# Kernel tuning notes

Hardware: AMD Instinct MI355X
Metric: run time of the kernel (lower is better)

Reference implementation:

```python
import jax, jax.numpy as jnp
import numpy as np

N = 8192          # mesh vertices
E = 49152         # directed edges (avg degree 6)
M = 25            # kernel_size per pseudo-dim
DIM = 3           # pseudo-coordinate dim
K = M ** DIM      # 15625 weight matrices per layer
S = 2 ** DIM      # 8 nonzero degree-1 B-spline products per edge
LC, UC = -0.22703196, 0.36853024   # curvature range
LM, UM = 1.2585511, 1.648841       # myelin range
R = 10.0
LAYER_DIMS = [(2, 32), (32, 64), (64, 64), (64, 32), (32, 1)]


def transform(x):
    # rescale curv/myelin channels into [-R, R] with clamping (matches torch masking)
    t0 = (x[:, 0] - LC) / (UC - LC) * (2.0 * R) - R
    t1 = (x[:, 1] - LM) / (UM - LM) * (2.0 * R) - R
    return jnp.stack([jnp.clip(t0, -R, R), jnp.clip(t1, -R, R)], axis=1)


def spline_basis(pseudo):
    # open B-spline, degree 1: v in [0, M-1); 8 corner products per edge
    v = pseudo * (M - 1)
    lo = jnp.floor(v)
    f = v - lo                                                    # [E, DIM]
    lo = lo.astype(jnp.int32)
    bits = (jnp.arange(S)[:, None] >> jnp.arange(DIM)[None, :]) & 1   # [S, DIM]
    oh = bits.astype(pseudo.dtype)
    basis = jnp.prod(oh[None] * f[:, None, :] + (1.0 - oh[None]) * (1.0 - f[:, None, :]), axis=-1)  # [E, S]
    strides = (M ** jnp.arange(DIM)).astype(jnp.int32)
    wi = jnp.sum((lo[:, None, :] + bits[None]) * strides[None, None, :], axis=-1)  # [E, S] kernel indices
    return basis, wi


def spline_conv(h, src, dst, basis, wi, W, root, bias):
    xj = h[src]                                             # [E, Fin] gather
    msg = jnp.zeros((xj.shape[0], W.shape[2]), h.dtype)
    for s in range(S):                                      # fixed 8-way basis loop
        msg = msg + basis[:, s, None] * jnp.einsum('ei,eio->eo', xj, W[wi[:, s]])
    agg = jax.ops.segment_sum(msg, dst, num_segments=N)     # scatter-sum (norm=False)
    return agg + h @ root + bias


def setup_inputs() -> dict:
    key = jax.random.key(0)
    ks = jax.random.split(key, 3 + 2 * len(LAYER_DIMS))
    inp = {
        "x": jax.random.normal(ks[0], (N, 2), dtype=jnp.float32),
        "edge_index": jax.random.randint(ks[1], (2, E), 0, N),
        "pseudo": jax.random.uniform(ks[2], (E, DIM), dtype=jnp.float32),
    }
    for i, (fi, fo) in enumerate(LAYER_DIMS):
        kw, kr = ks[3 + 2 * i], ks[4 + 2 * i]
        inp[f"W{i+1}"] = jax.random.normal(kw, (K, fi, fo), dtype=jnp.float32) / np.float32(np.sqrt(fi * S))
        inp[f"root{i+1}"] = jax.random.normal(kr, (fi, fo), dtype=jnp.float32) / np.float32(np.sqrt(fi))
        inp[f"b{i+1}"] = jnp.zeros((fo,), dtype=jnp.float32)
    return inp


def reference(x, edge_index, pseudo, W1, root1, b1, W2, root2, b2, W3, root3, b3,
              W4, root4, b4, W5, root5, b5):
    src, dst = edge_index[0], edge_index[1]
    basis, wi = spline_basis(pseudo)   # shared across all 5 layers, as in the torch model
    h = transform(x)
    for W, r, b in ((W1, root1, b1), (W2, root2, b2), (W3, root3, b3),
                    (W4, root4, b4), (W5, root5, b5)):
        h = jax.nn.elu(spline_conv(h, src, dst, basis, wi, W, r, b))
    return h.reshape(-1)
```

## Files before the change

### kernel.cpp

```cpp
#include <hip/hip_runtime.h>
#include <math.h>

#define NV 8192
#define EV 49152
#define KK 15625

typedef __attribute__((ext_vector_type(8))) short bf16x8;
typedef __attribute__((ext_vector_type(4))) float f32x4;

__device__ __forceinline__ unsigned short bf16rne(float x) {
    unsigned u = __float_as_uint(x);
    unsigned r = u + 0x7FFFu + ((u >> 16) & 1u);
    return (unsigned short)(r >> 16);
}
__device__ __forceinline__ float bf16tof(unsigned short h) {
    return __uint_as_float(((unsigned)h) << 16);
}

__device__ __forceinline__ void edge_frac(const float* __restrict__ pseudo, int e,
                                          float f[3], int lo[3]) {
#pragma unroll
    for (int j = 0; j < 3; ++j) {
        float v = pseudo[e * 3 + j] * 24.0f;
        float fl = floorf(v);
        int l = (int)fl;
        l = l < 0 ? 0 : (l > 23 ? 23 : l);
        lo[j] = l;
        f[j] = v - (float)l;
    }
}

__global__ void transform_kernel(const float* __restrict__ x, float* __restrict__ h0) {
    int n = blockIdx.x * blockDim.x + threadIdx.x;
    if (n >= NV) return;
    const float LC = -0.22703196f, UC = 0.36853024f;
    const float LM = 1.2585511f, UM = 1.648841f;
    const float R = 10.0f;
    float t0 = (x[n * 2 + 0] - LC) / (UC - LC) * (2.0f * R) - R;
    float t1 = (x[n * 2 + 1] - LM) / (UM - LM) * (2.0f * R) - R;
    h0[n * 2 + 0] = fminf(fmaxf(t0, -R), R);
    h0[n * 2 + 1] = fminf(fmaxf(t1, -R), R);
}

__global__ void hist_kernel(const float* __restrict__ pseudo, int* __restrict__ counts) {
    int e = blockIdx.x * blockDim.x + threadIdx.x;
    if (e >= EV) return;
    float f[3]; int lo[3];
    edge_frac(pseudo, e, f, lo);
#pragma unroll
    for (int s = 0; s < 8; ++s) {
        int wi = (lo[0] + (s & 1)) + 25 * (lo[1] + ((s >> 1) & 1)) + 625 * (lo[2] + ((s >> 2) & 1));
        atomicAdd(&counts[wi], 1);
    }
}

__global__ void scan_kernel(const int* __restrict__ counts, int* __restrict__ offsets,
                            int* __restrict__ cursor) {
    __shared__ int sums[256];
    const int CH = 62;
    int t = threadIdx.x;
    int base = t * CH;
    int s = 0;
    for (int i = 0; i < CH; ++i) {
        int idx = base + i;
        if (idx < KK) s += counts[idx];
    }
    sums[t] = s;
    __syncthreads();
    for (int d = 1; d < 256; d <<= 1) {
        int v = (t >= d) ? sums[t - d] : 0;
        __syncthreads();
        sums[t] += v;
        __syncthreads();
    }
    int run = (t > 0) ? sums[t - 1] : 0;
    for (int i = 0; i < CH; ++i) {
        int idx = base + i;
        if (idx < KK) {
            offsets[idx] = run;
            cursor[idx] = run;
            run += counts[idx];
        }
    }
    if (t == 255) offsets[KK] = run;
}

__global__ void scatter_kernel(const float* __restrict__ pseudo, const int* __restrict__ ei,
                               int* __restrict__ cursor,
                               int2* __restrict__ pair_sb, int* __restrict__ pair_dst) {
    int e = blockIdx.x * blockDim.x + threadIdx.x;
    if (e >= EV) return;
    float f[3]; int lo[3];
    edge_frac(pseudo, e, f, lo);
    int src = ei[e];
    int dst = ei[EV + e];
#pragma unroll
    for (int s = 0; s < 8; ++s) {
        float b = ((s & 1) ? f[0] : 1.0f - f[0]) *
                  (((s >> 1) & 1) ? f[1] : 1.0f - f[1]) *
                  (((s >> 2) & 1) ? f[2] : 1.0f - f[2]);
        int wi = (lo[0] + (s & 1)) + 25 * (lo[1] + ((s >> 1) & 1)) + 625 * (lo[2] + ((s >> 2) & 1));
        int pos = atomicAdd(&cursor[wi], 1);
        pair_sb[pos] = make_int2(src, __float_as_int(b));
        pair_dst[pos] = dst;
    }
}

template <int FIN, int FOUT>
__global__ __launch_bounds__(256) void conv_mfma(
    const float* __restrict__ h, const float* __restrict__ W,
    const int* __restrict__ offsets, const int2* __restrict__ pair_sb,
    const int* __restrict__ pair_dst, float* __restrict__ agg) {
    constexpr int KT = FIN / 32;
    constexpr int NT = FOUT / 16;
    int w = threadIdx.x >> 6;
    int lane = threadIdx.x & 63;
    int k = blockIdx.x * 4 + w;
    if (k >= KK) return;
    int start = offsets[k];
    int n = offsets[k + 1] - start;
    if (n <= 0) return;
    int l15 = lane & 15;
    int lg = lane >> 4;

    const float* Wk = W + (size_t)k * (FIN * FOUT);
    bf16x8 Bh[NT][KT], Bl[NT][KT];
#pragma unroll
    for (int n0 = 0; n0 < NT; ++n0)
#pragma unroll
        for (int k0 = 0; k0 < KT; ++k0)
#pragma unroll
            for (int i = 0; i < 8; ++i) {
                float wv = Wk[(size_t)(k0 * 32 + lg * 8 + i) * FOUT + n0 * 16 + l15];
                unsigned short hi = bf16rne(wv);
                unsigned short lo = bf16rne(wv - bf16tof(hi));
                Bh[n0][k0][i] = (short)hi;
                Bl[n0][k0][i] = (short)lo;
            }

    for (int m0 = 0; m0 < n; m0 += 16) {
        int ra = m0 + l15;
        bool va = ra < n;
        int2 sb = pair_sb[start + (va ? ra : 0)];
        float b = va ? __int_as_float(sb.y) : 0.0f;
        const float* xr = h + (size_t)sb.x * FIN + lg * 8;

        f32x4 acc[NT];
#pragma unroll
        for (int n0 = 0; n0 < NT; ++n0) acc[n0] = (f32x4){0.f, 0.f, 0.f, 0.f};

#pragma unroll
        for (int k0 = 0; k0 < KT; ++k0) {
            float4 v0 = *(const float4*)(xr + k0 * 32);
            float4 v1 = *(const float4*)(xr + k0 * 32 + 4);
            float xv[8] = {v0.x * b, v0.y * b, v0.z * b, v0.w * b,
                           v1.x * b, v1.y * b, v1.z * b, v1.w * b};
            bf16x8 Ah, Al;
#pragma unroll
            for (int i = 0; i < 8; ++i) {
                unsigned short hi = bf16rne(xv[i]);
                unsigned short lo = bf16rne(xv[i] - bf16tof(hi));
                Ah[i] = (short)hi;
                Al[i] = (short)lo;
            }
#pragma unroll
            for (int n0 = 0; n0 < NT; ++n0) {
                acc[n0] = __builtin_amdgcn_mfma_f32_16x16x32_bf16(Ah, Bh[n0][k0], acc[n0], 0, 0, 0);
                acc[n0] = __builtin_amdgcn_mfma_f32_16x16x32_bf16(Ah, Bl[n0][k0], acc[n0], 0, 0, 0);
                acc[n0] = __builtin_amdgcn_mfma_f32_16x16x32_bf16(Al, Bh[n0][k0], acc[n0], 0, 0, 0);
            }
        }

#pragma unroll
        for (int j = 0; j < 4; ++j) {
            int rm = m0 + lg * 4 + j;
            if (rm < n) {
                int d = pair_dst[start + rm];
#pragma unroll
                for (int n0 = 0; n0 < NT; ++n0)
                    atomicAdd(&agg[(size_t)d * FOUT + n0 * 16 + l15], acc[n0][j]);
            }
        }
    }
}

__global__ __launch_bounds__(256) void conv_l1(
    const float* __restrict__ h, const float* __restrict__ W,
    const int* __restrict__ offsets, const int2* __restrict__ pair_sb,
    const int* __restrict__ pair_dst, float* __restrict__ agg) {
    int w = threadIdx.x >> 6;
    int lane = threadIdx.x & 63;
    int k = blockIdx.x * 4 + w;
    if (k >= KK) return;
    int start = offsets[k];
    int n = offsets[k + 1] - start;
    if (n <= 0) return;
    int o = lane & 31;
    int g = lane >> 5;
    const float* Wk = W + (size_t)k * 64;
    float w0 = Wk[o], w1 = Wk[32 + o];
    const float2* h2 = (const float2*)h;
    for (int r = g; r < n; r += 2) {
        int2 sb = pair_sb[start + r];
        float b = __int_as_float(sb.y);
        int dst = pair_dst[start + r];
        float2 xv = h2[sb.x];
        atomicAdd(&agg[(size_t)dst * 32 + o], b * (xv.x * w0 + xv.y * w1));
    }
}

__global__ __launch_bounds__(256) void conv_f1(
    const float* __restrict__ h, const float* __restrict__ W,
    const int* __restrict__ offsets, const int2* __restrict__ pair_sb,
    const int* __restrict__ pair_dst, float* __restrict__ agg) {
    int w = threadIdx.x >> 6;
    int lane = threadIdx.x & 63;
    int k = blockIdx.x * 4 + w;
    if (k >= KK) return;
    int start = offsets[k];
    int n = offsets[k + 1] - start;
    if (n <= 0) return;
    int i = lane & 31;
    int g = lane >> 5;
    float wk = W[(size_t)k * 32 + i];
    for (int r = g; r < n; r += 2) {
        int2 sb = pair_sb[start + r];
        float b = __int_as_float(sb.y);
        int dst = pair_dst[start + r];
        float val = h[(size_t)sb.x * 32 + i] * wk * b;
#pragma unroll
        for (int d = 16; d >= 1; d >>= 1) val += __shfl_xor(val, d, 32);
        if (i == 0) atomicAdd(&agg[dst], val);
    }
}

template <int FIN, int FOUT>
__global__ void node_kernel(const float* __restrict__ h, const float* __restrict__ agg,
                            const float* __restrict__ root, const float* __restrict__ bias,
                            float* __restrict__ hout) {
    int idx = blockIdx.x * blockDim.x + threadIdx.x;
    if (idx >= NV * FOUT) return;
    int n = idx / FOUT, o = idx % FOUT;
    float acc = agg[idx] + bias[o];
#pragma unroll
    for (int i = 0; i < FIN; ++i) acc += h[n * FIN + i] * root[i * FOUT + o];
    hout[idx] = acc > 0.0f ? acc : expm1f(acc);
}

extern "C" void kernel_launch(void* const* d_in, const int* in_sizes, int n_in,
                              void* d_out, int out_size, void* d_ws, size_t ws_size,
                              hipStream_t stream) {
    const float* x      = (const float*)d_in[0];
    const int*   ei     = (const int*)d_in[1];
    const float* pseudo = (const float*)d_in[2];
    const float* W1 = (const float*)d_in[3];
    const float* r1 = (const float*)d_in[4];
    const float* b1 = (const float*)d_in[5];
    const float* W2 = (const float*)d_in[6];
    const float* r2 = (const float*)d_in[7];
    const float* b2 = (const float*)d_in[8];
    const float* W3 = (const float*)d_in[9];
    const float* r3 = (const float*)d_in[10];
    const float* b3 = (const float*)d_in[11];
    const float* W4 = (const float*)d_in[12];
    const float* r4 = (const float*)d_in[13];
    const float* b4 = (const float*)d_in[14];
    const float* W5 = (const float*)d_in[15];
    const float* r5 = (const float*)d_in[16];
    const float* b5 = (const float*)d_in[17];

    char* ws = (char*)d_ws;
    size_t off = 0;
    auto alloc = [&](size_t bytes) {
        void* p = ws + off;
        off += (bytes + 255) & ~(size_t)255;
        return p;
    };
    int*   counts   = (int*)alloc(KK * sizeof(int));
    int*   offsets  = (int*)alloc((KK + 1) * sizeof(int));
    int*   cursor   = (int*)alloc(KK * sizeof(int));
    int2*  pair_sb  = (int2*)alloc((size_t)EV * 8 * sizeof(int2));
    int*   pair_dst = (int*)alloc((size_t)EV * 8 * sizeof(int));
    float* hA       = (float*)alloc((size_t)NV * 64 * sizeof(float));
    float* hB       = (float*)alloc((size_t)NV * 64 * sizeof(float));
    float* agg      = (float*)alloc((size_t)NV * 64 * sizeof(float));

    const int CGRID = (KK + 3) / 4;

    hipMemsetAsync(counts, 0, KK * sizeof(int), stream);
    transform_kernel<<<(NV + 255) / 256, 256, 0, stream>>>(x, hA);
    hist_kernel<<<(EV + 255) / 256, 256, 0, stream>>>(pseudo, counts);
    scan_kernel<<<1, 256, 0, stream>>>(counts, offsets, cursor);
    scatter_kernel<<<(EV + 255) / 256, 256, 0, stream>>>(pseudo, ei, cursor, pair_sb, pair_dst);

    hipMemsetAsync(agg, 0, (size_t)NV * 32 * sizeof(float), stream);
    conv_l1<<<CGRID, 256, 0, stream>>>(hA, W1, offsets, pair_sb, pair_dst, agg);
    node_kernel<2, 32><<<(NV * 32 + 255) / 256, 256, 0, stream>>>(hA, agg, r1, b1, hB);

    hipMemsetAsync(agg, 0, (size_t)NV * 64 * sizeof(float), stream);
    conv_mfma<32, 64><<<CGRID, 256, 0, stream>>>(hB, W2, offsets, pair_sb, pair_dst, agg);
    node_kernel<32, 64><<<(NV * 64 + 255) / 256, 256, 0, stream>>>(hB, agg, r2, b2, hA);

    hipMemsetAsync(agg, 0, (size_t)NV * 64 * sizeof(float), stream);
    conv_mfma<64, 64><<<CGRID, 256, 0, stream>>>(hA, W3, offsets, pair_sb, pair_dst, agg);
    node_kernel<64, 64><<<(NV * 64 + 255) / 256, 256, 0, stream>>>(hA, agg, r3, b3, hB);

    hipMemsetAsync(agg, 0, (size_t)NV * 32 * sizeof(float), stream);
    conv_mfma<64, 32><<<CGRID, 256, 0, stream>>>(hB, W4, offsets, pair_sb, pair_dst, agg);
    node_kernel<64, 32><<<(NV * 32 + 255) / 256, 256, 0, stream>>>(hB, agg, r4, b4, hA);

    hipMemsetAsync(agg, 0, (size_t)NV * sizeof(float), stream);
    conv_f1<<<CGRID, 256, 0, stream>>>(hA, W5, offsets, pair_sb, pair_dst, agg);
    node_kernel<32, 1><<<(NV + 255) / 256, 256, 0, stream>>>(hA, agg, r5, b5, (float*)d_out);
}
```

Baseline: 509.9 us.

## Split conv output columns across waves and fold agg zeroing into kernels

Each MFMA conv wave now handles one 16-column output slice of a kernel matrix, so the work for one weight matrix spreads over several waves. Per-wave register use drops and more waves are in flight, at the cost of each wave reloading the same source rows and pair lists. The memsets are removed: a prep kernel zeroes counts and agg alongside the transform, and each node kernel clears agg after reading it. This cuts launch count but makes every node kernel touch the full 64-wide agg buffer.

New measurement: 518.9 us. No clear change (+1.8%).

```diff
diff --git a/kernel.cpp b/kernel.cpp
--- a/kernel.cpp
+++ b/kernel.cpp
@@ -30,16 +30,20 @@
     }
 }
 
-__global__ void transform_kernel(const float* __restrict__ x, float* __restrict__ h0) {
-    int n = blockIdx.x * blockDim.x + threadIdx.x;
-    if (n >= NV) return;
-    const float LC = -0.22703196f, UC = 0.36853024f;
-    const float LM = 1.2585511f, UM = 1.648841f;
-    const float R = 10.0f;
-    float t0 = (x[n * 2 + 0] - LC) / (UC - LC) * (2.0f * R) - R;
-    float t1 = (x[n * 2 + 1] - LM) / (UM - LM) * (2.0f * R) - R;
-    h0[n * 2 + 0] = fminf(fmaxf(t0, -R), R);
-    h0[n * 2 + 1] = fminf(fmaxf(t1, -R), R);
+__global__ void prep_kernel(const float* __restrict__ x, float* __restrict__ h0,
+                            int* __restrict__ counts, float* __restrict__ agg) {
+    int gt = blockIdx.x * blockDim.x + threadIdx.x;
+    if (gt < NV) {
+        const float LC = -0.22703196f, UC = 0.36853024f;
+        const float LM = 1.2585511f, UM = 1.648841f;
+        const float R = 10.0f;
+        float t0 = (x[gt * 2 + 0] - LC) / (UC - LC) * (2.0f * R) - R;
+        float t1 = (x[gt * 2 + 1] - LM) / (UM - LM) * (2.0f * R) - R;
+        h0[gt * 2 + 0] = fminf(fmaxf(t0, -R), R);
+        h0[gt * 2 + 1] = fminf(fmaxf(t1, -R), R);
+    }
+    if (gt < KK) counts[gt] = 0;
+    if (gt < NV * 64) agg[gt] = 0.0f;
 }
 
 __global__ void hist_kernel(const float* __restrict__ pseudo, int* __restrict__ counts) {
@@ -107,15 +111,17 @@
 }
 
 template <int FIN, int FOUT>
-__global__ __launch_bounds__(256) void conv_mfma(
+__global__ __launch_bounds__(256) void conv_v5(
     const float* __restrict__ h, const float* __restrict__ W,
     const int* __restrict__ offsets, const int2* __restrict__ pair_sb,
     const int* __restrict__ pair_dst, float* __restrict__ agg) {
     constexpr int KT = FIN / 32;
     constexpr int NT = FOUT / 16;
+    constexpr int BPB = 4 / NT;
     int w = threadIdx.x >> 6;
     int lane = threadIdx.x & 63;
-    int k = blockIdx.x * 4 + w;
+    int nslice = w % NT;
+    int k = blockIdx.x * BPB + w / NT;
     if (k >= KK) return;
     int start = offsets[k];
     int n = offsets[k + 1] - start;
@@ -123,32 +129,30 @@
     int l15 = lane & 15;
     int lg = lane >> 4;
 
-    const float* Wk = W + (size_t)k * (FIN * FOUT);
-    bf16x8 Bh[NT][KT], Bl[NT][KT];
-#pragma unroll
-    for (int n0 = 0; n0 < NT; ++n0)
-#pragma unroll
-        for (int k0 = 0; k0 < KT; ++k0)
-#pragma unroll
-            for (int i = 0; i < 8; ++i) {
-                float wv = Wk[(size_t)(k0 * 32 + lg * 8 + i) * FOUT + n0 * 16 + l15];
-                unsigned short hi = bf16rne(wv);
-                unsigned short lo = bf16rne(wv - bf16tof(hi));
-                Bh[n0][k0][i] = (short)hi;
-                Bl[n0][k0][i] = (short)lo;
-            }
+    const float* Wk = W + (size_t)k * (FIN * FOUT) + nslice * 16 + l15;
+    bf16x8 Bh[KT], Bl[KT];
+#pragma unroll
+    for (int k0 = 0; k0 < KT; ++k0)
+#pragma unroll
+        for (int i = 0; i < 8; ++i) {
+            float wv = Wk[(size_t)(k0 * 32 + lg * 8 + i) * FOUT];
+            unsigned short hi = bf16rne(wv);
+            unsigned short lo = bf16rne(wv - bf16tof(hi));
+            Bh[k0][i] = (short)hi;
+            Bl[k0][i] = (short)lo;
+        }
+
+    const int2* psb = pair_sb + start;
+    const int* pdst = pair_dst + start;
 
     for (int m0 = 0; m0 < n; m0 += 16) {
         int ra = m0 + l15;
         bool va = ra < n;
-        int2 sb = pair_sb[start + (va ? ra : 0)];
+        int2 sb = psb[va ? ra : 0];
         float b = va ? __int_as_float(sb.y) : 0.0f;
         const float* xr = h + (size_t)sb.x * FIN + lg * 8;
 
-        f32x4 acc[NT];
-#pragma unroll
-        for (int n0 = 0; n0 < NT; ++n0) acc[n0] = (f32x4){0.f, 0.f, 0.f, 0.f};
-
+        f32x4 acc = (f32x4){0.f, 0.f, 0.f, 0.f};
 #pragma unroll
         for (int k0 = 0; k0 < KT; ++k0) {
             float4 v0 = *(const float4*)(xr + k0 * 32);
@@ -163,22 +167,17 @@
                 Ah[i] = (short)hi;
                 Al[i] = (short)lo;
             }
-#pragma unroll
-            for (int n0 = 0; n0 < NT; ++n0) {
-                acc[n0] = __builtin_amdgcn_mfma_f32_16x16x32_bf16(Ah, Bh[n0][k0], acc[n0], 0, 0, 0);
-                acc[n0] = __builtin_amdgcn_mfma_f32_16x16x32_bf16(Ah, Bl[n0][k0], acc[n0], 0, 0, 0);
-                acc[n0] = __builtin_amdgcn_mfma_f32_16x16x32_bf16(Al, Bh[n0][k0], acc[n0], 0, 0, 0);
-            }
+            acc = __builtin_amdgcn_mfma_f32_16x16x32_bf16(Ah, Bh[k0], acc, 0, 0, 0);
+            acc = __builtin_amdgcn_mfma_f32_16x16x32_bf16(Ah, Bl[k0], acc, 0, 0, 0);
+            acc = __builtin_amdgcn_mfma_f32_16x16x32_bf16(Al, Bh[k0], acc, 0, 0, 0);
         }
 
 #pragma unroll
         for (int j = 0; j < 4; ++j) {
             int rm = m0 + lg * 4 + j;
             if (rm < n) {
-                int d = pair_dst[start + rm];
-#pragma unroll
-                for (int n0 = 0; n0 < NT; ++n0)
-                    atomicAdd(&agg[(size_t)d * FOUT + n0 * 16 + l15], acc[n0][j]);
+                int d = pdst[rm];
+                atomicAdd(&agg[(size_t)d * FOUT + nslice * 16 + l15], acc[j]);
             }
         }
     }
@@ -235,16 +234,19 @@
 }
 
 template <int FIN, int FOUT>
-__global__ void node_kernel(const float* __restrict__ h, const float* __restrict__ agg,
+__global__ void node_kernel(const float* __restrict__ h, float* __restrict__ agg,
                             const float* __restrict__ root, const float* __restrict__ bias,
                             float* __restrict__ hout) {
     int idx = blockIdx.x * blockDim.x + threadIdx.x;
-    if (idx >= NV * FOUT) return;
-    int n = idx / FOUT, o = idx % FOUT;
-    float acc = agg[idx] + bias[o];
-#pragma unroll
-    for (int i = 0; i < FIN; ++i) acc += h[n * FIN + i] * root[i * FOUT + o];
-    hout[idx] = acc > 0.0f ? acc : expm1f(acc);
+    if (idx >= NV * 64) return;
+    if (idx < NV * FOUT) {
+        int n = idx / FOUT, o = idx % FOUT;
+        float acc = agg[idx] + bias[o];
+#pragma unroll
+        for (int i = 0; i < FIN; ++i) acc += h[n * FIN + i] * root[i * FOUT + o];
+        hout[idx] = acc > 0.0f ? acc : expm1f(acc);
+    }
+    agg[idx] = 0.0f;
 }
 
 extern "C" void kernel_launch(void* const* d_in, const int* in_sizes, int n_in,
@@ -285,31 +287,25 @@
     float* hB       = (float*)alloc((size_t)NV * 64 * sizeof(float));
     float* agg      = (float*)alloc((size_t)NV * 64 * sizeof(float));
 
-    const int CGRID = (KK + 3) / 4;
-
-    hipMemsetAsync(counts, 0, KK * sizeof(int), stream);
-    transform_kernel<<<(NV + 255) / 256, 256, 0, stream>>>(x, hA);
+    const int NGRID = (NV * 64 + 255) / 256;
+
+    prep_kernel<<<NGRID, 256, 0, stream>>>(x, hA, counts, agg);
     hist_kernel<<<(EV + 255) / 256, 256, 0, stream>>>(pseudo, counts);
     scan_kernel<<<1, 256, 0, stream>>>(counts, offsets, cursor);
     scatter_kernel<<<(EV + 255) / 256, 256, 0, stream>>>(pseudo, ei, cursor, pair_sb, pair_dst);
 
-    hipMemsetAsync(agg, 0, (size_t)NV * 32 * sizeof(float), stream);
-    conv_l1<<<CGRID, 256, 0, stream>>>(hA, W1, offsets, pair_sb, pair_dst, agg);
-    node_kernel<2, 32><<<(NV * 32 + 255) / 256, 256, 0, stream>>>(hA, agg, r1, b1, hB);
-
-    hipMemsetAsync(agg, 0, (size_t)NV * 64 * sizeof(float), stream);
-    conv_mfma<32, 64><<<CGRID, 256, 0, stream>>>(hB, W2, offsets, pair_sb, pair_dst, agg);
-    node_kernel<32, 64><<<(NV * 64 + 255) / 256, 256, 0, stream>>>(hB, agg, r2, b2, hA);
-
-    hipMemsetAsync(agg, 0, (size_t)NV * 64 * sizeof(float), stream);
-    conv_mfma<64, 64><<<CGRID, 256, 0, stream>>>(hA, W3, offsets, pair_sb, pair_dst, agg);
-    node_kernel<64, 64><<<(NV * 64 + 255) / 256, 256, 0, stream>>>(hA, agg, r3, b3, hB);
-
-    hipMemsetAsync(agg, 0, (size_t)NV * 32 * sizeof(float), stream);
-    conv_mfma<64, 32><<<CGRID, 256, 0, stream>>>(hB, W4, offsets, pair_sb, pair_dst, agg);
-    node_kernel<64, 32><<<(NV * 32 + 255) / 256, 256, 0, stream>>>(hB, agg, r4, b4, hA);
-
-    hipMemsetAsync(agg, 0, (size_t)NV * sizeof(float), stream);
-    conv_f1<<<CGRID, 256, 0, stream>>>(hA, W5, offsets, pair_sb, pair_dst, agg);
-    node_kernel<32, 1><<<(NV + 255) / 256, 256, 0, stream>>>(hA, agg, r5, b5, (float*)d_out);
-}
+    conv_l1<<<(KK + 3) / 4, 256, 0, stream>>>(hA, W1, offsets, pair_sb, pair_dst, agg);
+    node_kernel<2, 32><<<NGRID, 256, 0, stream>>>(hA, agg, r1, b1, hB);
+
+    conv_v5<32, 64><<<KK, 256, 0, stream>>>(hB, W2, offsets, pair_sb, pair_dst, agg);
+    node_kernel<32, 64><<<NGRID, 256, 0, stream>>>(hB, agg, r2, b2, hA);
+
+    conv_v5<64, 64><<<KK, 256, 0, stream>>>(hA, W3, offsets, pair_sb, pair_dst, agg);
+    node_kernel<64, 64><<<NGRID, 256, 0, stream>>>(hA, agg, r3, b3, hB);
+
+    conv_v5<64, 32><<<(KK + 1) / 2, 256, 0, stream>>>(hB, W4, offsets, pair_sb, pair_dst, agg);
+    node_kernel<64, 32><<<NGRID, 256, 0, stream>>>(hB, agg, r4, b4, hA);
+
+    conv_f1<<<(KK + 3) / 4, 256, 0, stream>>>(hA, W5, offsets, pair_sb, pair_dst, agg);
+    node_kernel<32, 1><<<NGRID, 256, 0, stream>>>(hA, agg, r5, b5, (float*)d_out);
+}
```
